# Kernel optimization log

Hardware: AMD Instinct MI355X
Metric: run time of the kernel (lower is better)

## Reference

```python
import jax, jax.numpy as jnp
import numpy as np

NODE_SIZE = 128
EDGE_SIZE = 20
CUTOFF = 5.0
N_NODES = 20000
N_EDGES = 600000


def silu(x):
    return x * jax.nn.sigmoid(x)


def setup_inputs() -> dict:
    key = jax.random.key(0)
    ks = jax.random.split(key, 20)
    d = NODE_SIZE
    inp = {
        "node_states_scalar": jax.random.normal(ks[0], (N_NODES, d), jnp.float32),
        "node_states_vector": jax.random.normal(ks[1], (N_NODES, 3, d), jnp.float32),
        "edge_states": jax.random.normal(ks[2], (N_EDGES, EDGE_SIZE), jnp.float32),
        "edge_vectors": jax.random.normal(ks[3], (N_EDGES, 3), jnp.float32),
        "edge_norms": jax.random.uniform(ks[4], (N_EDGES, 1), jnp.float32),
        "edge_index": jax.random.randint(ks[5], (N_EDGES, 2), 0, N_NODES, jnp.int64 if jax.config.jax_enable_x64 else jnp.int32),
        # parameters, stored as [in, out] so y = x @ W + b
        "Wf": jax.random.normal(ks[6], (EDGE_SIZE, 3 * d), jnp.float32) * 0.05,
        "bf": jnp.zeros((3 * d,), jnp.float32),
        "Wm1": jax.random.normal(ks[7], (d, d), jnp.float32) * 0.05,
        "bm1": jnp.zeros((d,), jnp.float32),
        "Wm2": jax.random.normal(ks[8], (d, 3 * d), jnp.float32) * 0.05,
        "bm2": jnp.zeros((3 * d,), jnp.float32),
        "WU": jax.random.normal(ks[9], (d, d), jnp.float32) * 0.05,
        "WV": jax.random.normal(ks[10], (d, d), jnp.float32) * 0.05,
        "Wa1": jax.random.normal(ks[11], (2 * d, d), jnp.float32) * 0.05,
        "ba1": jnp.zeros((d,), jnp.float32),
        "Wa2": jax.random.normal(ks[12], (d, 3 * d), jnp.float32) * 0.05,
        "ba2": jnp.zeros((3 * d,), jnp.float32),
    }
    return inp


def reference(node_states_scalar, node_states_vector, edge_states, edge_vectors,
              edge_norms, edge_index, Wf, bf, Wm1, bm1, Wm2, bm2, WU, WV,
              Wa1, ba1, Wa2, ba2):
    d = NODE_SIZE
    n = node_states_scalar.shape[0]

    # --- message function ---
    # cosine cutoff: 0.5*(cos(pi*r/cutoff)+1) for r < cutoff, else 0
    fc = 0.5 * (jnp.cos(jnp.pi * edge_norms / CUTOFF) + 1.0)
    fc = jnp.where(edge_norms < CUTOFF, fc, 0.0)                      # [E,1]
    filter_weight = (edge_states @ Wf + bf) * fc                      # [E,3d]
    scalar_output = silu(node_states_scalar @ Wm1 + bm1) @ Wm2 + bm2  # [N,3d]

    src = edge_index[:, 0]
    dst = edge_index[:, 1]
    filter_output = filter_weight * scalar_output[src]                # [E,3d]
    gate_nodes = filter_output[:, :d]
    gate_edges = filter_output[:, d:2 * d]
    messages_scalar = filter_output[:, 2 * d:]

    gated_node_vec = node_states_vector[src] * gate_nodes[:, None, :]     # [E,3,d]
    gated_edge_vec = gate_edges[:, None, :] * edge_vectors[:, :, None]    # [E,3,d]
    messages_vector = gated_node_vec + gated_edge_vec

    ds_m = jax.ops.segment_sum(messages_scalar, dst, num_segments=n)  # [N,d]
    dv_m = jax.ops.segment_sum(messages_vector, dst, num_segments=n)  # [N,3,d]

    s = node_states_scalar + ds_m
    v = node_states_vector + dv_m

    # --- node state update ---
    Uv = jnp.einsum('nvd,de->nve', v, WU)
    Vv = jnp.einsum('nvd,de->nve', v, WV)
    Vv_sq = jnp.sum(Vv ** 2, axis=1)                                  # [N,d]
    a = silu(jnp.concatenate([s, Vv_sq], axis=1) @ Wa1 + ba1) @ Wa2 + ba2
    a_ss, a_sv, a_vv = a[:, :d], a[:, d:2 * d], a[:, 2 * d:]
    ip = jnp.sum(Uv * Vv, axis=1)                                     # [N,d]

    s = s + a_ss + a_sv * ip
    v = v + a_vv[:, None, :] * Uv
    return (s, v)
```

## Files before the change

kernel.cpp:

```cpp
#include <hip/hip_runtime.h>

#define ND 128
#define ESZ 20
#define NN 20000
#define NE 600000
#define PI_F 3.14159265358979323846f
#define CUT 5.0f

using short8 = __attribute__((ext_vector_type(8))) short;
using f32x4  = __attribute__((ext_vector_type(4))) float;
using hh2    = __attribute__((ext_vector_type(2))) _Float16;

__device__ __forceinline__ float silu_f(float x) { return x / (1.0f + __expf(-x)); }

__device__ __forceinline__ unsigned short f2bf(float x) {
    unsigned u = __float_as_uint(x);
    unsigned r = (u + 0x7FFFu + ((u >> 16) & 1u)) >> 16;
    return (unsigned short)r;
}
__device__ __forceinline__ float bf2f(unsigned short h) {
    return __uint_as_float(((unsigned)h) << 16);
}
__device__ __forceinline__ unsigned pack2h(float x, float y) {
    _Float16 a = (_Float16)x, b = (_Float16)y;
    unsigned short ua = __builtin_bit_cast(unsigned short, a);
    unsigned short ub = __builtin_bit_cast(unsigned short, b);
    return (unsigned)ua | ((unsigned)ub << 16);
}
__device__ __forceinline__ float dot2u(unsigned a, hh2 b, float acc) {
    return __builtin_amdgcn_fdot2(__builtin_bit_cast(hh2, a), b, acc, false);
}

__device__ __forceinline__ void pack_w(const float* __restrict__ W,
                                       unsigned short* __restrict__ P,
                                       int s, int K, int N) {
    int k = s / N, n = s - k * N;
    int dst = ((((n >> 4) * (K >> 5) + (k >> 5)) * 64) +
               (((k >> 3) & 3) << 4) + (n & 15)) * 8 + (k & 7);
    P[dst] = f2bf(W[s]);
}

#define R0 1920000L
#define R1 (R0 + 180224L)
#define R2 (R1 + 4224L)
#define R3 (R2 + 600000L)
#define R4 (R3 + 600000L)

__global__ __launch_bounds__(256) void k_front(
    const float4* __restrict__ ns4, const float4* __restrict__ nsv4,
    const float* __restrict__ es, const float* __restrict__ enorm,
    const int* __restrict__ eidx,
    const float* __restrict__ Wf, const float* __restrict__ bfb,
    const float* __restrict__ Wm1, const float* __restrict__ Wm2,
    const float* __restrict__ WU, const float* __restrict__ WV,
    const float* __restrict__ Wa1, const float* __restrict__ Wa2,
    float4* __restrict__ outs4, float4* __restrict__ outv4,
    ushort4* __restrict__ nsb4, unsigned* __restrict__ gnh,
    unsigned short* __restrict__ p1, unsigned short* __restrict__ p2,
    unsigned short* __restrict__ pU, unsigned short* __restrict__ pV,
    unsigned short* __restrict__ pa1, unsigned short* __restrict__ pa2,
    unsigned* __restrict__ wfh, unsigned* __restrict__ eshu,
    int* __restrict__ counts) {
    long gid = (long)blockIdx.x * 256 + threadIdx.x;
    if (gid < R0) {
        long i = gid;
        const long S4 = (long)NN * ND / 4;
        if (i < S4) {
            float4 v = ns4[i];
            outs4[i] = v;
            ushort4 h; h.x = f2bf(v.x); h.y = f2bf(v.y); h.z = f2bf(v.z); h.w = f2bf(v.w);
            nsb4[i] = h;
        }
        float4 w = nsv4[i];
        outv4[i] = w;
        unsigned short* gs = (unsigned short*)gnh;
        long b = i * 4;
        gs[(b + 0) * 2 + 1] = f2bf(w.x);
        gs[(b + 1) * 2 + 1] = f2bf(w.y);
        gs[(b + 2) * 2 + 1] = f2bf(w.z);
        gs[(b + 3) * 2 + 1] = f2bf(w.w);
    } else if (gid < R1) {
        int i = (int)(gid - R0);
        if      (i <  16384) pack_w(Wm1, p1, i,          128, 128);
        else if (i <  65536) pack_w(Wm2, p2, i - 16384,  128, 384);
        else if (i <  81920) pack_w(WU,  pU, i - 65536,  128, 128);
        else if (i <  98304) pack_w(WV,  pV, i - 81920,  128, 128);
        else if (i < 131072) pack_w(Wa1, pa1, i - 98304, 256, 128);
        else                 pack_w(Wa2, pa2, i - 131072,128, 384);
    } else if (gid < R2) {
        int j = (int)(gid - R1);
        int p = j / 384, cc = j - p * 384;
        float a = 0.f, b = 0.f;
        if (p < 10) { a = Wf[(2 * p) * 384 + cc]; b = Wf[(2 * p + 1) * 384 + cc]; }
        else if (p == 10) { a = bfb[cc]; }
        wfh[p * 384 + cc] = pack2h(a, b);
    } else if (gid < R3) {
        int e = (int)(gid - R2);
        float nrm = enorm[e];
        float fc = (nrm < CUT) ? 0.5f * (__cosf(PI_F * nrm * (1.0f / CUT)) + 1.0f) : 0.0f;
        const float* er = es + (long)e * ESZ;
        unsigned* dst = eshu + (long)e * 12;
#pragma unroll
        for (int p = 0; p < 10; ++p)
            dst[p] = pack2h(er[2 * p] * fc, er[2 * p + 1] * fc);
        dst[10] = pack2h(fc, 0.f);
        dst[11] = 0u;
    } else if (gid < R4) {
        int e = (int)(gid - R3);
        atomicAdd(&counts[eidx[2 * e + 1]], 1);
    }
}

#define SCAN_T 1024
__global__ __launch_bounds__(SCAN_T) void k_scan(const int* __restrict__ counts,
                                                 int* __restrict__ offsets,
                                                 int* __restrict__ cursor) {
    __shared__ int part[SCAN_T];
    const int t = threadIdx.x;
    const int CPT = (NN + SCAN_T - 1) / SCAN_T;
    const int base = t * CPT;
    int sum = 0;
    for (int i = 0; i < CPT; ++i) {
        int idx = base + i;
        if (idx < NN) sum += counts[idx];
    }
    part[t] = sum;
    __syncthreads();
    for (int off = 1; off < SCAN_T; off <<= 1) {
        int v = (t >= off) ? part[t - off] : 0;
        __syncthreads();
        part[t] += v;
        __syncthreads();
    }
    int run = (t == 0) ? 0 : part[t - 1];
    for (int i = 0; i < CPT; ++i) {
        int idx = base + i;
        if (idx < NN) {
            offsets[idx] = run;
            cursor[idx] = run;
            run += counts[idx];
        }
    }
    if (t == SCAN_T - 1) offsets[NN] = run;
}

#define SCAT_B 2344
__global__ __launch_bounds__(256) void k_sm(
    const int* __restrict__ eidx, int* __restrict__ cursor, int* __restrict__ perm,
    const unsigned short* __restrict__ nsb,
    const unsigned short* __restrict__ Wm1p, const float* __restrict__ bm1,
    const unsigned short* __restrict__ Wm2p, const float* __restrict__ bm2,
    unsigned* __restrict__ gnh) {
    __shared__ unsigned short lsh[4][16][136];
    if (blockIdx.x < SCAT_B) {
        int e = blockIdx.x * 256 + threadIdx.x;
        if (e < NE) {
            int pos = atomicAdd(&cursor[eidx[2 * e + 1]], 1);
            perm[pos] = e;
        }
        return;
    }
    const int lane = threadIdx.x & 63;
    const int wv = threadIdx.x >> 6;
    const int wid = (blockIdx.x - SCAT_B) * 4 + wv;
    const int m0 = wid * 16;
    if (m0 >= NN) return;
    const int ml = lane & 15, q = lane >> 4;

    short8 a1[4];
#pragma unroll
    for (int kb = 0; kb < 4; ++kb)
        a1[kb] = *(const short8*)(nsb + (long)(m0 + ml) * ND + kb * 32 + q * 8);

#pragma unroll
    for (int nt = 0; nt < 8; ++nt) {
        float b = bm1[nt * 16 + ml];
        f32x4 acc = {b, b, b, b};
#pragma unroll
        for (int kb = 0; kb < 4; ++kb) {
            short8 bf = *(const short8*)(Wm1p + ((nt * 4 + kb) * 64 + lane) * 8);
            acc = __builtin_amdgcn_mfma_f32_16x16x32_bf16(a1[kb], bf, acc, 0, 0, 0);
        }
#pragma unroll
        for (int r = 0; r < 4; ++r)
            lsh[wv][q * 4 + r][nt * 16 + ml] = f2bf(silu_f(acc[r]));
    }
    __syncthreads();

    short8 a2[4];
#pragma unroll
    for (int kb = 0; kb < 4; ++kb)
        a2[kb] = *(const short8*)(&lsh[wv][ml][kb * 32 + q * 8]);

    unsigned short* gs = (unsigned short*)gnh;
#pragma unroll
    for (int nt = 0; nt < 24; ++nt) {
        float b = bm2[nt * 16 + ml];
        f32x4 acc = {b, b, b, b};
#pragma unroll
        for (int kb = 0; kb < 4; ++kb) {
            short8 bf = *(const short8*)(Wm2p + ((nt * 4 + kb) * 64 + lane) * 8);
            acc = __builtin_amdgcn_mfma_f32_16x16x32_bf16(a2[kb], bf, acc, 0, 0, 0);
        }
#pragma unroll
        for (int r = 0; r < 4; ++r) {
            long idx = (long)(m0 + q * 4 + r) * 384 + nt * 16 + ml;
            gs[idx * 2] = f2bf(acc[r]);
        }
    }
}

#define NGRP 8192
#define RUN ((NE + NGRP - 1) / NGRP)

#define LOADE(S, i_) {                                                        \
    int e_ = __builtin_amdgcn_readfirstlane(perm[i_]);                        \
    src##S = __builtin_amdgcn_readfirstlane(eidx[2 * e_]);                    \
    dst##S = __builtin_amdgcn_readfirstlane(eidx[2 * e_ + 1]);                \
    ev0##S = evec[3 * e_ + 0];                                                \
    ev1##S = evec[3 * e_ + 1];                                                \
    ev2##S = evec[3 * e_ + 2];                                                \
    const uint4* ep_ = esh4 + (long)e_ * 3;                                   \
    q0##S = ep_[0]; q1##S = ep_[1]; q2##S = ep_[2];                           \
    const unsigned* gp_ = gnh + (long)src##S * 384;                           \
    x0##S = gp_[t]; x1##S = gp_[128 + t]; x2##S = gp_[256 + t];               \
}

#define FLUSH() {                                                             \
    atomicAdd(&out_s[(long)cur_dst * ND + t], as);                            \
    atomicAdd(&out_v[(long)cur_dst * 384 + 0 * ND + t], av0);                 \
    atomicAdd(&out_v[(long)cur_dst * 384 + 1 * ND + t], av1);                 \
    atomicAdd(&out_v[(long)cur_dst * 384 + 2 * ND + t], av2);                 \
}

#define COMPE(S) {                                                            \
    if (dst##S != cur_dst) {                                                  \
        if (cur_dst >= 0) FLUSH();                                            \
        cur_dst = dst##S;                                                     \
        as = 0.f; av0 = 0.f; av1 = 0.f; av2 = 0.f;                            \
    }                                                                         \
    unsigned ea_[11] = {q0##S.x, q0##S.y, q0##S.z, q0##S.w,                   \
                        q1##S.x, q1##S.y, q1##S.z, q1##S.w,                   \
                        q2##S.x, q2##S.y, q2##S.z};                           \
    float f0 = 0.f, f1 = 0.f, f2 = 0.f;                                       \
    _Pragma("unroll")                                                         \
    for (int p = 0; p < 11; ++p) {                                            \
        f0 = dot2u(ea_[p], wf[p][0], f0);                                     \
        f1 = dot2u(ea_[p], wf[p][1], f1);                                     \
        f2 = dot2u(ea_[p], wf[p][2], f2);                                     \
    }                                                                         \
    f0 *= __uint_as_float(x0##S << 16);                                       \
    f1 *= __uint_as_float(x1##S << 16);                                       \
    f2 *= __uint_as_float(x2##S << 16);                                       \
    as  += f2;                                                                \
    av0 += __uint_as_float(x0##S & 0xffff0000u) * f0 + f1 * ev0##S;           \
    av1 += __uint_as_float(x1##S & 0xffff0000u) * f0 + f1 * ev1##S;           \
    av2 += __uint_as_float(x2##S & 0xffff0000u) * f0 + f1 * ev2##S;           \
}

__global__ __launch_bounds__(256, 4) void k_edge5(
    const uint4* __restrict__ esh4, const float* __restrict__ evec,
    const int* __restrict__ eidx, const int* __restrict__ perm,
    const unsigned* __restrict__ wfh, const unsigned* __restrict__ gnh,
    float* __restrict__ out_s, float* __restrict__ out_v) {
    const int t = threadIdx.x & 127;
    const int grp = blockIdx.x * 2 + (threadIdx.x >> 7);
    const int beg = grp * RUN;
    const int end = (beg + RUN < NE) ? beg + RUN : NE;
    if (beg >= end) return;

    hh2 wf[11][3];
#pragma unroll
    for (int p = 0; p < 11; ++p)
#pragma unroll
        for (int c = 0; c < 3; ++c)
            wf[p][c] = __builtin_bit_cast(hh2, wfh[p * 384 + c * 128 + t]);

    int srcA, dstA, srcB, dstB;
    float ev0A, ev1A, ev2A, ev0B, ev1B, ev2B;
    uint4 q0A, q1A, q2A, q0B, q1B, q2B;
    unsigned x0A, x1A, x2A, x0B, x1B, x2B;

    LOADE(A, beg);
    LOADE(B, beg + 1);

    int cur_dst = -1;
    float as = 0.f, av0 = 0.f, av1 = 0.f, av2 = 0.f;

    for (int i = beg; i < end; i += 2) {
        COMPE(A);
        int ia = (i + 2 < end) ? i + 2 : end - 1;
        LOADE(A, ia);
        COMPE(B);
        int ib = (i + 3 < end) ? i + 3 : end - 1;
        LOADE(B, ib);
    }
    FLUSH();
}

__global__ __launch_bounds__(256) void k_uvm(
    const float* __restrict__ out_v, const float* __restrict__ out_s,
    const unsigned short* __restrict__ WUp, const unsigned short* __restrict__ WVp,
    unsigned short* __restrict__ Uvh, unsigned short* __restrict__ cat,
    float* __restrict__ ipb) {
    const int lane = threadIdx.x & 63;
    const int wid = blockIdx.x * 4 + (threadIdx.x >> 6);
    const int m0 = wid * 16;
    if (m0 >= NN) return;
    const int ml = lane & 15, q = lane >> 4;

#pragma unroll
    for (int j = 0; j < 32; ++j) {
        int idx = j * 64 + lane;
        int n = m0 + (idx >> 7), c = idx & 127;
        cat[(long)n * 256 + c] = f2bf(out_s[(long)n * 128 + c]);
    }

    short8 av[3][4];
#pragma unroll
    for (int ax = 0; ax < 3; ++ax)
#pragma unroll
        for (int kb = 0; kb < 4; ++kb) {
            const float* p = out_v + (long)(m0 + ml) * 384 + ax * 128 + kb * 32 + q * 8;
            float4 x = *(const float4*)p;
            float4 y = *(const float4*)(p + 4);
            short8 s;
            s[0] = (short)f2bf(x.x); s[1] = (short)f2bf(x.y);
            s[2] = (short)f2bf(x.z); s[3] = (short)f2bf(x.w);
            s[4] = (short)f2bf(y.x); s[5] = (short)f2bf(y.y);
            s[6] = (short)f2bf(y.z); s[7] = (short)f2bf(y.w);
            av[ax][kb] = s;
        }

#pragma unroll
    for (int nt = 0; nt < 8; ++nt) {
        f32x4 u0 = {0.f,0.f,0.f,0.f}, u1 = u0, u2 = u0;
        f32x4 v0 = u0, v1 = u0, v2 = u0;
#pragma unroll
        for (int kb = 0; kb < 4; ++kb) {
            short8 bu = *(const short8*)(WUp + ((nt * 4 + kb) * 64 + lane) * 8);
            short8 bv = *(const short8*)(WVp + ((nt * 4 + kb) * 64 + lane) * 8);
            u0 = __builtin_amdgcn_mfma_f32_16x16x32_bf16(av[0][kb], bu, u0, 0, 0, 0);
            u1 = __builtin_amdgcn_mfma_f32_16x16x32_bf16(av[1][kb], bu, u1, 0, 0, 0);
            u2 = __builtin_amdgcn_mfma_f32_16x16x32_bf16(av[2][kb], bu, u2, 0, 0, 0);
            v0 = __builtin_amdgcn_mfma_f32_16x16x32_bf16(av[0][kb], bv, v0, 0, 0, 0);
            v1 = __builtin_amdgcn_mfma_f32_16x16x32_bf16(av[1][kb], bv, v1, 0, 0, 0);
            v2 = __builtin_amdgcn_mfma_f32_16x16x32_bf16(av[2][kb], bv, v2, 0, 0, 0);
        }
        const int c = nt * 16 + ml;
#pragma unroll
        for (int r = 0; r < 4; ++r) {
            long grow = m0 + q * 4 + r;
            float vs  = v0[r] * v0[r] + v1[r] * v1[r] + v2[r] * v2[r];
            float ipv = u0[r] * v0[r] + u1[r] * v1[r] + u2[r] * v2[r];
            cat[grow * 256 + 128 + c] = f2bf(vs);
            ipb[grow * 128 + c] = ipv;
            Uvh[(grow * 3 + 0) * 128 + c] = f2bf(u0[r]);
            Uvh[(grow * 3 + 1) * 128 + c] = f2bf(u1[r]);
            Uvh[(grow * 3 + 2) * 128 + c] = f2bf(u2[r]);
        }
    }
}

__global__ __launch_bounds__(256) void k_att(
    const unsigned short* __restrict__ cat,
    const unsigned short* __restrict__ Wa1p, const float* __restrict__ ba1,
    const unsigned short* __restrict__ Wa2p, const float* __restrict__ ba2,
    const float* __restrict__ ipb, const unsigned short* __restrict__ Uvh,
    float* __restrict__ out_s, float* __restrict__ out_v) {
    const int lane = threadIdx.x & 63;
    const int wv = threadIdx.x >> 6;
    const int wid = blockIdx.x * 4 + wv;
    const int m0 = wid * 16;
    if (m0 >= NN) return;
    const int ml = lane & 15, q = lane >> 4;
    __shared__ unsigned short lsh[4][16][136];

    short8 a1[8];
#pragma unroll
    for (int kb = 0; kb < 8; ++kb)
        a1[kb] = *(const short8*)(cat + (long)(m0 + ml) * 256 + kb * 32 + q * 8);

#pragma unroll
    for (int nt = 0; nt < 8; ++nt) {
        float b = ba1[nt * 16 + ml];
        f32x4 acc = {b, b, b, b};
#pragma unroll
        for (int kb = 0; kb < 8; ++kb) {
            short8 bf = *(const short8*)(Wa1p + ((nt * 8 + kb) * 64 + lane) * 8);
            acc = __builtin_amdgcn_mfma_f32_16x16x32_bf16(a1[kb], bf, acc, 0, 0, 0);
        }
#pragma unroll
        for (int r = 0; r < 4; ++r)
            lsh[wv][q * 4 + r][nt * 16 + ml] = f2bf(silu_f(acc[r]));
    }
    __syncthreads();

    short8 h[4];
#pragma unroll
    for (int kb = 0; kb < 4; ++kb)
        h[kb] = *(const short8*)(&lsh[wv][ml][kb * 32 + q * 8]);

#pragma unroll
    for (int nt = 0; nt < 8; ++nt) {
        float b0 = ba2[nt * 16 + ml];
        float b1 = ba2[128 + nt * 16 + ml];
        f32x4 aS = {b0, b0, b0, b0};
        f32x4 aG = {b1, b1, b1, b1};
#pragma unroll
        for (int kb = 0; kb < 4; ++kb) {
            short8 bS = *(const short8*)(Wa2p + (((nt) * 4 + kb) * 64 + lane) * 8);
            short8 bG = *(const short8*)(Wa2p + (((nt + 8) * 4 + kb) * 64 + lane) * 8);
            aS = __builtin_amdgcn_mfma_f32_16x16x32_bf16(h[kb], bS, aS, 0, 0, 0);
            aG = __builtin_amdgcn_mfma_f32_16x16x32_bf16(h[kb], bG, aG, 0, 0, 0);
        }
#pragma unroll
        for (int r = 0; r < 4; ++r) {
            long grow = m0 + q * 4 + r;
            long o = grow * 128 + nt * 16 + ml;
            float ipv = ipb[o];
            out_s[o] = out_s[o] + aS[r] + aG[r] * ipv;
        }
    }

#pragma unroll
    for (int nt = 0; nt < 8; ++nt) {
        float b2 = ba2[256 + nt * 16 + ml];
        f32x4 aV = {b2, b2, b2, b2};
#pragma unroll
        for (int kb = 0; kb < 4; ++kb) {
            short8 bV = *(const short8*)(Wa2p + (((nt + 16) * 4 + kb) * 64 + lane) * 8);
            aV = __builtin_amdgcn_mfma_f32_16x16x32_bf16(h[kb], bV, aV, 0, 0, 0);
        }
#pragma unroll
        for (int r = 0; r < 4; ++r) {
            long grow = m0 + q * 4 + r;
            int c = nt * 16 + ml;
#pragma unroll
            for (int ax = 0; ax < 3; ++ax) {
                float u = bf2f(Uvh[(grow * 3 + ax) * 128 + c]);
                long o = grow * 384 + ax * 128 + c;
                out_v[o] = out_v[o] + aV[r] * u;
            }
        }
    }
}

extern "C" void kernel_launch(void* const* d_in, const int* in_sizes, int n_in,
                              void* d_out, int out_size, void* d_ws, size_t ws_size,
                              hipStream_t stream) {
    const float* ns    = (const float*)d_in[0];
    const float* nsv   = (const float*)d_in[1];
    const float* es    = (const float*)d_in[2];
    const float* evec  = (const float*)d_in[3];
    const float* enorm = (const float*)d_in[4];
    const int*   eidx  = (const int*)d_in[5];
    const float* Wf    = (const float*)d_in[6];
    const float* bfb   = (const float*)d_in[7];
    const float* Wm1   = (const float*)d_in[8];
    const float* bm1   = (const float*)d_in[9];
    const float* Wm2   = (const float*)d_in[10];
    const float* bm2   = (const float*)d_in[11];
    const float* WU    = (const float*)d_in[12];
    const float* WV    = (const float*)d_in[13];
    const float* Wa1   = (const float*)d_in[14];
    const float* ba1   = (const float*)d_in[15];
    const float* Wa2   = (const float*)d_in[16];
    const float* ba2   = (const float*)d_in[17];

    float* out_s = (float*)d_out;
    float* out_v = out_s + (size_t)NN * ND;

    char* w = (char*)d_ws;
    unsigned short* p1  = (unsigned short*)(w + 0);
    unsigned short* p2  = (unsigned short*)(w + 32768);
    unsigned short* pU  = (unsigned short*)(w + 131072);
    unsigned short* pV  = (unsigned short*)(w + 163840);
    unsigned short* pa1 = (unsigned short*)(w + 196608);
    unsigned short* pa2 = (unsigned short*)(w + 262144);
    unsigned* wfh = (unsigned*)(w + 360448);
    int* counts = (int*)(w + 377344);
    int* offs   = (int*)(w + 457344);
    int* cursor = (int*)(w + 537408);
    int* perm   = (int*)(w + 617408);
    char* u0 = w + 3017408;
    unsigned* gnh       = (unsigned*)(u0);
    unsigned short* nsb = (unsigned short*)(u0 + 30720000);
    unsigned* eshu      = (unsigned*)(u0 + 35840000);
    unsigned short* Uvh = (unsigned short*)(u0);
    unsigned short* cat = (unsigned short*)(u0 + 15360000);
    float*          ipb = (float*)(u0 + 25600000);

    hipMemsetAsync(counts, 0, (size_t)NN * sizeof(int), stream);
    k_front<<<(int)((R4 + 255) / 256), 256, 0, stream>>>(
        (const float4*)ns, (const float4*)nsv, es, enorm, eidx, Wf, bfb,
        Wm1, Wm2, WU, WV, Wa1, Wa2,
        (float4*)out_s, (float4*)out_v, (ushort4*)nsb, gnh,
        p1, p2, pU, pV, pa1, pa2, wfh, eshu, counts);
    k_scan<<<1, SCAN_T, 0, stream>>>(counts, offs, cursor);
    k_sm<<<SCAT_B + 313, 256, 0, stream>>>(eidx, cursor, perm,
                                           nsb, p1, bm1, p2, bm2, gnh);
    k_edge5<<<NGRP / 2, 256, 0, stream>>>((const uint4*)eshu, evec, eidx, perm,
                                          wfh, gnh, out_s, out_v);
    k_uvm<<<313, 256, 0, stream>>>(out_v, out_s, pU, pV, Uvh, cat, ipb);
    k_att<<<313, 256, 0, stream>>>(cat, pa1, ba1, pa2, ba2, ipb, Uvh,
                                   out_s, out_v);
}
```

Baseline: 575.3 us.

## Scatter packed per-edge records in dst order and stage them via LDS

```diff
diff --git a/kernel.cpp b/kernel.cpp
--- a/kernel.cpp
+++ b/kernel.cpp
@@ -44,11 +44,9 @@
 #define R1 (R0 + 180224L)
 #define R2 (R1 + 4224L)
 #define R3 (R2 + 600000L)
-#define R4 (R3 + 600000L)
 
 __global__ __launch_bounds__(256) void k_front(
     const float4* __restrict__ ns4, const float4* __restrict__ nsv4,
-    const float* __restrict__ es, const float* __restrict__ enorm,
     const int* __restrict__ eidx,
     const float* __restrict__ Wf, const float* __restrict__ bfb,
     const float* __restrict__ Wm1, const float* __restrict__ Wm2,
@@ -59,8 +57,7 @@
     unsigned short* __restrict__ p1, unsigned short* __restrict__ p2,
     unsigned short* __restrict__ pU, unsigned short* __restrict__ pV,
     unsigned short* __restrict__ pa1, unsigned short* __restrict__ pa2,
-    unsigned* __restrict__ wfh, unsigned* __restrict__ eshu,
-    int* __restrict__ counts) {
+    unsigned* __restrict__ wfh, int* __restrict__ counts) {
     long gid = (long)blockIdx.x * 256 + threadIdx.x;
     if (gid < R0) {
         long i = gid;
@@ -96,17 +93,6 @@
         wfh[p * 384 + cc] = pack2h(a, b);
     } else if (gid < R3) {
         int e = (int)(gid - R2);
-        float nrm = enorm[e];
-        float fc = (nrm < CUT) ? 0.5f * (__cosf(PI_F * nrm * (1.0f / CUT)) + 1.0f) : 0.0f;
-        const float* er = es + (long)e * ESZ;
-        unsigned* dst = eshu + (long)e * 12;
-#pragma unroll
-        for (int p = 0; p < 10; ++p)
-            dst[p] = pack2h(er[2 * p] * fc, er[2 * p + 1] * fc);
-        dst[10] = pack2h(fc, 0.f);
-        dst[11] = 0u;
-    } else if (gid < R4) {
-        int e = (int)(gid - R3);
         atomicAdd(&counts[eidx[2 * e + 1]], 1);
     }
 }
@@ -146,7 +132,9 @@
 
 #define SCAT_B 2344
 __global__ __launch_bounds__(256) void k_sm(
-    const int* __restrict__ eidx, int* __restrict__ cursor, int* __restrict__ perm,
+    const int* __restrict__ eidx, int* __restrict__ cursor,
+    const float* __restrict__ es, const float* __restrict__ enorm,
+    const float* __restrict__ evec, unsigned* __restrict__ rec,
     const unsigned short* __restrict__ nsb,
     const unsigned short* __restrict__ Wm1p, const float* __restrict__ bm1,
     const unsigned short* __restrict__ Wm2p, const float* __restrict__ bm2,
@@ -155,8 +143,24 @@
     if (blockIdx.x < SCAT_B) {
         int e = blockIdx.x * 256 + threadIdx.x;
         if (e < NE) {
-            int pos = atomicAdd(&cursor[eidx[2 * e + 1]], 1);
-            perm[pos] = e;
+            int s  = eidx[2 * e];
+            int dd = eidx[2 * e + 1];
+            float nrm = enorm[e];
+            float fc = (nrm < CUT) ? 0.5f * (__cosf(PI_F * nrm * (1.0f / CUT)) + 1.0f) : 0.0f;
+            const float* er = es + (long)e * ESZ;
+            unsigned qv[11];
+#pragma unroll
+            for (int p = 0; p < 10; ++p)
+                qv[p] = pack2h(er[2 * p] * fc, er[2 * p + 1] * fc);
+            qv[10] = pack2h(fc, 0.f);
+            float e0 = evec[3 * e + 0], e1 = evec[3 * e + 1], e2 = evec[3 * e + 2];
+            int pos = atomicAdd(&cursor[dd], 1);
+            uint4* rp = (uint4*)rec + (long)pos * 4;
+            rp[0] = make_uint4((unsigned)s, (unsigned)dd,
+                               __float_as_uint(e0), __float_as_uint(e1));
+            rp[1] = make_uint4(__float_as_uint(e2), qv[0], qv[1], qv[2]);
+            rp[2] = make_uint4(qv[3], qv[4], qv[5], qv[6]);
+            rp[3] = make_uint4(qv[7], qv[8], qv[9], qv[10]);
         }
         return;
     }
@@ -213,16 +217,22 @@
 #define NGRP 8192
 #define RUN ((NE + NGRP - 1) / NGRP)
 
-#define LOADE(S, i_) {                                                        \
-    int e_ = __builtin_amdgcn_readfirstlane(perm[i_]);                        \
-    src##S = __builtin_amdgcn_readfirstlane(eidx[2 * e_]);                    \
-    dst##S = __builtin_amdgcn_readfirstlane(eidx[2 * e_ + 1]);                \
-    ev0##S = evec[3 * e_ + 0];                                                \
-    ev1##S = evec[3 * e_ + 1];                                                \
-    ev2##S = evec[3 * e_ + 2];                                                \
-    const uint4* ep_ = esh4 + (long)e_ * 3;                                   \
-    q0##S = ep_[0]; q1##S = ep_[1]; q2##S = ep_[2];                           \
-    const unsigned* gp_ = gnh + (long)src##S * 384;                           \
+#define SL(R, k) { R = *(const uint4*)(rec + ((long)beg + (long)(k) * 16) * 16 + lane * 4); }
+#define SW(R, k) { *(uint4*)&eb[wv][(k) & 1][lane * 4] = R; }
+
+#define LREAD(S, l_) {                                                        \
+    int ll = ((l_) < nl) ? (l_) : nl - 1;                                     \
+    const unsigned* ep_ = &eb[wv][(ll >> 4) & 1][(ll & 15) << 4];             \
+    m0##S = *(const uint4*)(ep_);                                             \
+    m1##S = *(const uint4*)(ep_ + 4);                                         \
+    m2##S = *(const uint4*)(ep_ + 8);                                         \
+    m3##S = *(const uint4*)(ep_ + 12);                                        \
+}
+
+#define LGATH(S) {                                                            \
+    int s_ = __builtin_amdgcn_readfirstlane((int)m0##S.x);                    \
+    dst##S = __builtin_amdgcn_readfirstlane((int)m0##S.y);                    \
+    const unsigned* gp_ = gnh + (long)s_ * 384;                               \
     x0##S = gp_[t]; x1##S = gp_[128 + t]; x2##S = gp_[256 + t];               \
 }
 
@@ -239,9 +249,9 @@
         cur_dst = dst##S;                                                     \
         as = 0.f; av0 = 0.f; av1 = 0.f; av2 = 0.f;                            \
     }                                                                         \
-    unsigned ea_[11] = {q0##S.x, q0##S.y, q0##S.z, q0##S.w,                   \
-                        q1##S.x, q1##S.y, q1##S.z, q1##S.w,                   \
-                        q2##S.x, q2##S.y, q2##S.z};                           \
+    unsigned ea_[11] = {m1##S.y, m1##S.z, m1##S.w,                            \
+                        m2##S.x, m2##S.y, m2##S.z, m2##S.w,                   \
+                        m3##S.x, m3##S.y, m3##S.z, m3##S.w};                  \
     float f0 = 0.f, f1 = 0.f, f2 = 0.f;                                       \
     _Pragma("unroll")                                                         \
     for (int p = 0; p < 11; ++p) {                                            \
@@ -252,22 +262,28 @@
     f0 *= __uint_as_float(x0##S << 16);                                       \
     f1 *= __uint_as_float(x1##S << 16);                                       \
     f2 *= __uint_as_float(x2##S << 16);                                       \
+    float ev0_ = __uint_as_float(m0##S.z);                                    \
+    float ev1_ = __uint_as_float(m0##S.w);                                    \
+    float ev2_ = __uint_as_float(m1##S.x);                                    \
     as  += f2;                                                                \
-    av0 += __uint_as_float(x0##S & 0xffff0000u) * f0 + f1 * ev0##S;           \
-    av1 += __uint_as_float(x1##S & 0xffff0000u) * f0 + f1 * ev1##S;           \
-    av2 += __uint_as_float(x2##S & 0xffff0000u) * f0 + f1 * ev2##S;           \
-}
-
-__global__ __launch_bounds__(256, 4) void k_edge5(
-    const uint4* __restrict__ esh4, const float* __restrict__ evec,
-    const int* __restrict__ eidx, const int* __restrict__ perm,
-    const unsigned* __restrict__ wfh, const unsigned* __restrict__ gnh,
+    av0 += __uint_as_float(x0##S & 0xffff0000u) * f0 + f1 * ev0_;             \
+    av1 += __uint_as_float(x1##S & 0xffff0000u) * f0 + f1 * ev1_;             \
+    av2 += __uint_as_float(x2##S & 0xffff0000u) * f0 + f1 * ev2_;             \
+}
+
+__global__ __launch_bounds__(256, 4) void k_edge6(
+    const unsigned* __restrict__ rec, const unsigned* __restrict__ wfh,
+    const unsigned* __restrict__ gnh,
     float* __restrict__ out_s, float* __restrict__ out_v) {
-    const int t = threadIdx.x & 127;
-    const int grp = blockIdx.x * 2 + (threadIdx.x >> 7);
+    __shared__ __align__(16) unsigned eb[4][2][256];
+    const int wv = threadIdx.x >> 6;
+    const int lane = threadIdx.x & 63;
+    const int grp = blockIdx.x * 2 + (wv >> 1);
+    const int t = ((wv & 1) << 6) | lane;
     const int beg = grp * RUN;
     const int end = (beg + RUN < NE) ? beg + RUN : NE;
     if (beg >= end) return;
+    const int nl = end - beg;
 
     hh2 wf[11][3];
 #pragma unroll
@@ -276,24 +292,33 @@
         for (int c = 0; c < 3; ++c)
             wf[p][c] = __builtin_bit_cast(hh2, wfh[p * 384 + c * 128 + t]);
 
-    int srcA, dstA, srcB, dstB;
-    float ev0A, ev1A, ev2A, ev0B, ev1B, ev2B;
-    uint4 q0A, q1A, q2A, q0B, q1B, q2B;
+    uint4 st0, st1;
+    uint4 m0A, m1A, m2A, m3A, m0B, m1B, m2B, m3B;
     unsigned x0A, x1A, x2A, x0B, x1B, x2B;
-
-    LOADE(A, beg);
-    LOADE(B, beg + 1);
+    int dstA, dstB;
+
+    SL(st0, 0); SL(st1, 1);
+    SW(st0, 0); SW(st1, 1);
+    SL(st0, 2);
+
+    LREAD(A, 0); LGATH(A);
+    LREAD(B, 1); LGATH(B);
 
     int cur_dst = -1;
     float as = 0.f, av0 = 0.f, av1 = 0.f, av2 = 0.f;
 
-    for (int i = beg; i < end; i += 2) {
+    for (int l = 0; l < nl; l += 2) {
+        if (l && !(l & 15)) {
+            int c = l >> 4;
+            if ((c + 1) & 1) { SW(st1, c + 1); SL(st0, c + 2); }
+            else             { SW(st0, c + 1); SL(st1, c + 2); }
+        }
         COMPE(A);
-        int ia = (i + 2 < end) ? i + 2 : end - 1;
-        LOADE(A, ia);
+        LREAD(A, l + 2);
         COMPE(B);
-        int ib = (i + 3 < end) ? i + 3 : end - 1;
-        LOADE(B, ib);
+        LGATH(A);
+        LREAD(B, l + 3);
+        LGATH(B);
     }
     FLUSH();
 }
@@ -482,26 +507,24 @@
     int* counts = (int*)(w + 377344);
     int* offs   = (int*)(w + 457344);
     int* cursor = (int*)(w + 537408);
-    int* perm   = (int*)(w + 617408);
-    char* u0 = w + 3017408;
+    unsigned* rec = (unsigned*)(w + 617408);
+    char* u0 = w + 39024576;
     unsigned* gnh       = (unsigned*)(u0);
     unsigned short* nsb = (unsigned short*)(u0 + 30720000);
-    unsigned* eshu      = (unsigned*)(u0 + 35840000);
     unsigned short* Uvh = (unsigned short*)(u0);
     unsigned short* cat = (unsigned short*)(u0 + 15360000);
     float*          ipb = (float*)(u0 + 25600000);
 
     hipMemsetAsync(counts, 0, (size_t)NN * sizeof(int), stream);
-    k_front<<<(int)((R4 + 255) / 256), 256, 0, stream>>>(
-        (const float4*)ns, (const float4*)nsv, es, enorm, eidx, Wf, bfb,
+    k_front<<<(int)((R3 + 255) / 256), 256, 0, stream>>>(
+        (const float4*)ns, (const float4*)nsv, eidx, Wf, bfb,
         Wm1, Wm2, WU, WV, Wa1, Wa2,
         (float4*)out_s, (float4*)out_v, (ushort4*)nsb, gnh,
-        p1, p2, pU, pV, pa1, pa2, wfh, eshu, counts);
+        p1, p2, pU, pV, pa1, pa2, wfh, counts);
     k_scan<<<1, SCAN_T, 0, stream>>>(counts, offs, cursor);
-    k_sm<<<SCAT_B + 313, 256, 0, stream>>>(eidx, cursor, perm,
+    k_sm<<<SCAT_B + 313, 256, 0, stream>>>(eidx, cursor, es, enorm, evec, rec,
                                            nsb, p1, bm1, p2, bm2, gnh);
-    k_edge5<<<NGRP / 2, 256, 0, stream>>>((const uint4*)eshu, evec, eidx, perm,
-                                          wfh, gnh, out_s, out_v);
+    k_edge6<<<NGRP / 2, 256, 0, stream>>>(rec, wfh, gnh, out_s, out_v);
     k_uvm<<<313, 256, 0, stream>>>(out_v, out_s, pU, pV, Uvh, cat, ipb);
     k_att<<<313, 256, 0, stream>>>(cat, pa1, ba1, pa2, ba2, ipb, Uvh,
                                    out_s, out_v);
```

After: 529.4 us. 1.09x faster.
